# Kernel optimization log

Hardware: AMD Instinct MI355X
Metric: run time of the kernel (lower is better)

## Reference

```python
import jax, jax.numpy as jnp
import numpy as np

T_STEPS = 1000
TEMP_SAMPLE = 0.1


def _cosine_schedule():
    # matches MBDDegradationImputation._cosine_beta_schedule (float64 then cast)
    s = 0.008
    x = np.linspace(0, T_STEPS, T_STEPS + 1, dtype=np.float64)
    ac = np.cos((x / T_STEPS + s) / (1 + s) * np.pi * 0.5) ** 2
    ac = ac / ac[0]
    betas = np.clip(1.0 - ac[1:] / ac[:-1], 0.0, 0.999)
    alphas = 1.0 - betas
    acp = np.cumprod(alphas)
    return (jnp.asarray(alphas, jnp.float32),
            jnp.asarray(acp, jnp.float32),
            jnp.asarray(np.sqrt(1.0 - acp), jnp.float32))


def setup_inputs() -> dict:
    key = jax.random.key(0)
    k = jax.random.split(key, 6)
    N, T, F = 2048, 512, 64
    Xbar_i = jax.random.normal(k[0], (T, F), jnp.float32)
    observed_data = jax.random.normal(k[1], (T, F), jnp.float32)
    time_points = jnp.linspace(0.0, 1.0, T, dtype=jnp.float32)
    mask = jax.random.uniform(k[2], (T, F)) > 0.3  # True = observed
    eps = jax.random.normal(k[3], (N, T, F), jnp.float32)
    deg_a = jax.random.normal(k[4], (F,), jnp.float32) * 0.1
    deg_b = jax.random.normal(k[5], (F,), jnp.float32) * 0.1
    return {"Xbar_i": Xbar_i, "observed_data": observed_data,
            "time_points": time_points, "mask": mask, "eps": eps,
            "deg_a": deg_a, "deg_b": deg_b, "i": 500}


def reference(Xbar_i, observed_data, time_points, mask, eps, deg_a, deg_b, i):
    alphas, acp, sigmas = _cosine_schedule()
    abar_i = acp[i]
    sigma_i = sigmas[i]
    alpha_i = alphas[i]
    abar_im1 = acp[i - 1]

    Yi = jnp.sqrt(abar_i) * Xbar_i  # (T, F)
    # candidate clean samples, clipped, observed positions restored
    X0s = jnp.clip(eps * sigma_i + Xbar_i, -1.0, 1.0)  # (N, T, F)
    cand = jnp.where(mask[None], observed_data[None], X0s)  # (N, T, F)

    # linear degradation model consistency: pred = a + b * t, score = -MSE
    pred = deg_a[None, :] + deg_b[None, :] * time_points[:, None]  # (T, F)
    scores = -jnp.mean((cand - pred[None]) ** 2, axis=(1, 2))  # (N,)

    std = jnp.maximum(jnp.std(scores, ddof=1), 1e-4)  # torch.std is unbiased
    logp0 = (scores - jnp.mean(scores)) / std / TEMP_SAMPLE
    weights = jax.nn.softmax(logp0)  # (N,)

    weighted = jnp.einsum('n,ntf->tf', weights, X0s)  # (T, F)
    # per-feature: missing positions get weighted combo; fully-observed
    # features are copied from observed_data; observed positions of
    # partially-missing features stay zero (faithful to the torch loop)
    feat_all = jnp.all(mask, axis=0)  # (F,)
    Xbar = jnp.where(~mask, weighted,
                     jnp.where(feat_all[None, :], observed_data, 0.0))

    score = (-Yi + jnp.sqrt(abar_i) * Xbar) / (1.0 - abar_i)
    Xim1 = (Yi + (1.0 - abar_i) * score) / jnp.sqrt(alpha_i)
    Xbar_im1 = Xim1 / jnp.sqrt(abar_im1)
    Xbar_im1 = jnp.where(mask, observed_data, Xbar_im1)
    return Xbar_im1
```

## Files before the change

kernel.cpp:

```cpp
#include <hip/hip_runtime.h>

typedef __attribute__((ext_vector_type(4))) int   i32x4;
typedef __attribute__((ext_vector_type(4))) float f32x4;

#define TF    32768
#define TF4   8192
#define NS    2048
#define NG    32
#define WCUT  1e-9f

__device__ __forceinline__ i32x4 mload4(const void* mask, int isI32, int idx4) {
  if (isI32) return ((const i32x4*)mask)[idx4];
  unsigned int w = ((const unsigned int*)mask)[idx4];
  i32x4 r;
  r[0] = (int)(w & 0xFFu);
  r[1] = (int)((w >> 8) & 0xFFu);
  r[2] = (int)((w >> 16) & 0xFFu);
  r[3] = (int)((w >> 24) & 0xFFu);
  return r;
}

__device__ __forceinline__ double ac_fn(int t) {
  const double s = 0.008;
  double c = cos(((double)t / 1000.0 + s) / (1.0 + s) * 1.5707963267948966);
  return c * c;
}
__device__ __forceinline__ double alpha_fn(int t) {
  double beta = 1.0 - ac_fn(t + 1) / ac_fn(t);
  beta = beta < 0.0 ? 0.0 : (beta > 0.999 ? 0.999 : beta);
  return 1.0 - beta;
}

__launch_bounds__(256)
__global__ void k1_fused(const int* __restrict__ ip,
                         const unsigned int* __restrict__ maskw,
                         const float* __restrict__ timep,
                         const float* __restrict__ dega,
                         const float* __restrict__ degb,
                         const float* __restrict__ xbar,
                         const float* __restrict__ obs,
                         const void* __restrict__ mask,
                         float* __restrict__ wsc,
                         float* __restrict__ sc, float* __restrict__ xq,
                         float* __restrict__ pq) {
  const int tid = threadIdx.x;
  __shared__ int badsh;
  __shared__ double prod[256];
  __shared__ float ssig;
  __shared__ int sIsI32;
  if (tid == 0) badsh = 0;
  __syncthreads();
  int bad = 0;
  for (int k = tid; k < TF4; k += 256)
    if (maskw[k] > 1u) bad = 1;
  if (bad) atomicOr(&badsh, 1);

  const int i = ip[0];
  double p = 1.0;
  for (int t = tid; t < i; t += 256) p *= alpha_fn(t);
  prod[tid] = p;
  __syncthreads();
  for (int s = 128; s > 0; s >>= 1) {
    if (tid < s) prod[tid] *= prod[tid + s];
    __syncthreads();
  }
  if (tid == 0) {
    double acp_im1 = prod[0];
    double ai = alpha_fn(i);
    double acp_i = acp_im1 * ai;
    float sig = (float)sqrt(1.0 - acp_i);
    ssig = sig;
    sIsI32 = badsh ? 0 : 1;
    if (blockIdx.x == 0) {
      wsc[0] = sig;
      wsc[1] = (float)acp_i;
      wsc[2] = (float)ai;
      wsc[3] = (float)acp_im1;
      ((int*)wsc)[8] = badsh ? 0 : 1;
    }
  }
  __syncthreads();
  const float sig = ssig;
  const int isI32 = sIsI32;

  const int pos4 = blockIdx.x * 256 + tid;
  const int t  = pos4 >> 4;
  const int f0 = (pos4 << 2) & 63;
  const float tv = timep[t];
  f32x4 da = *(const f32x4*)(dega + f0);
  f32x4 db = *(const f32x4*)(degb + f0);
  f32x4 x  = ((const f32x4*)xbar)[pos4];
  f32x4 o  = ((const f32x4*)obs)[pos4];
  i32x4 m  = mload4(mask, isI32, pos4);

  f32x4 scv, xqv, pqv;
  #pragma unroll
  for (int c = 0; c < 4; ++c) {
    const float pr = fmaf(db[c], tv, da[c]);
    const bool mm = m[c] != 0;
    scv[c] = mm ? 0.f : sig;
    xqv[c] = mm ? 0.f : x[c];
    pqv[c] = mm ? (o[c] - pr) : pr;
  }
  ((f32x4*)sc)[pos4] = scv;
  ((f32x4*)xq)[pos4] = xqv;
  ((f32x4*)pq)[pos4] = pqv;
}

__launch_bounds__(256)
__global__ void k2_scores(const float* __restrict__ eps,
                          const float* __restrict__ sc,
                          const float* __restrict__ xq,
                          const float* __restrict__ pq,
                          double* __restrict__ pscore) {
  const int tid = threadIdx.x;
  const int n0 = blockIdx.x * 4;
  const int kq = blockIdx.y;
  const int kbeg = kq * (TF4 / 4);
  const f32x4* e4 = (const f32x4*)eps;
  const f32x4* sc4 = (const f32x4*)sc;
  const f32x4* xq4 = (const f32x4*)xq;
  const f32x4* pq4 = (const f32x4*)pq;

  double acc[4] = {0.0, 0.0, 0.0, 0.0};
  #pragma unroll 2
  for (int k = kbeg + tid; k < kbeg + TF4 / 4; k += 512) {
    const int k1 = k + 256;
    f32x4 sv0 = sc4[k],  xv0 = xq4[k],  pv0 = pq4[k];
    f32x4 sv1 = sc4[k1], xv1 = xq4[k1], pv1 = pq4[k1];
    #pragma unroll
    for (int r = 0; r < 4; ++r) {
      const size_t row = (size_t)(n0 + r) * TF4;
      f32x4 e0 = e4[row + k];
      f32x4 e1 = e4[row + k1];
      float s = 0.f;
      #pragma unroll
      for (int c = 0; c < 4; ++c) {
        float v = fmaf(e0[c], sv0[c], xv0[c]);
        v = fminf(fmaxf(v, -1.f), 1.f);
        float d = v - pv0[c];
        s = fmaf(d, d, s);
      }
      #pragma unroll
      for (int c = 0; c < 4; ++c) {
        float v = fmaf(e1[c], sv1[c], xv1[c]);
        v = fminf(fmaxf(v, -1.f), 1.f);
        float d = v - pv1[c];
        s = fmaf(d, d, s);
      }
      acc[r] += (double)s;
    }
  }
  __shared__ double red[4 * 256];
  #pragma unroll
  for (int r = 0; r < 4; ++r) red[r * 256 + tid] = acc[r];
  __syncthreads();
  for (int s = 128; s > 0; s >>= 1) {
    if (tid < s) {
      #pragma unroll
      for (int r = 0; r < 4; ++r) red[r * 256 + tid] += red[r * 256 + tid + s];
    }
    __syncthreads();
  }
  if (tid < 4) pscore[kq * NS + n0 + tid] = red[tid * 256];
}

__launch_bounds__(256)
__global__ void k3_softmax(const double* __restrict__ pscore,
                           float* __restrict__ wsc,
                           int* __restrict__ cidx, float* __restrict__ cw) {
  const int tid = threadIdx.x;
  __shared__ double red[256];

  float s[8];
  #pragma unroll
  for (int j = 0; j < 8; ++j) {
    int n = tid + 256 * j;
    double t = pscore[n] + pscore[NS + n] + pscore[2 * NS + n] + pscore[3 * NS + n];
    s[j] = -(float)(t * (1.0 / 32768.0));
  }
  double t = 0.0;
  #pragma unroll
  for (int j = 0; j < 8; ++j) t += (double)s[j];
  red[tid] = t; __syncthreads();
  for (int st = 128; st > 0; st >>= 1) { if (tid < st) red[tid] += red[tid + st]; __syncthreads(); }
  const float mean = (float)(red[0] * (1.0 / 2048.0));
  __syncthreads();
  double v = 0.0;
  #pragma unroll
  for (int j = 0; j < 8; ++j) { float d = s[j] - mean; v += (double)d * (double)d; }
  red[tid] = v; __syncthreads();
  for (int st = 128; st > 0; st >>= 1) { if (tid < st) red[tid] += red[tid + st]; __syncthreads(); }
  float stdv = (float)sqrt(red[0] / 2047.0);
  stdv = fmaxf(stdv, 1e-4f);
  const float inv = 10.0f / stdv;
  float lp[8];
  double mx = -1e300;
  #pragma unroll
  for (int j = 0; j < 8; ++j) { lp[j] = (s[j] - mean) * inv; mx = fmax(mx, (double)lp[j]); }
  __syncthreads();
  red[tid] = mx; __syncthreads();
  for (int st = 128; st > 0; st >>= 1) { if (tid < st) red[tid] = fmax(red[tid], red[tid + st]); __syncthreads(); }
  const float M = (float)red[0];
  __syncthreads();
  float ev[8]; double es = 0.0;
  #pragma unroll
  for (int j = 0; j < 8; ++j) { ev[j] = expf(lp[j] - M); es += (double)ev[j]; }
  red[tid] = es; __syncthreads();
  for (int st = 128; st > 0; st >>= 1) { if (tid < st) red[tid] += red[tid + st]; __syncthreads(); }
  const float invS = (float)(1.0 / red[0]);

  float w[8]; int keep[8]; int c = 0;
  #pragma unroll
  for (int j = 0; j < 8; ++j) {
    w[j] = ev[j] * invS;
    keep[j] = w[j] > WCUT;
    c += keep[j];
  }
  __shared__ int cnt[256];
  cnt[tid] = c; __syncthreads();
  for (int off = 1; off < 256; off <<= 1) {
    int vv = (tid >= off) ? cnt[tid - off] : 0;
    __syncthreads();
    cnt[tid] += vv;
    __syncthreads();
  }
  int base = cnt[tid] - c;
  #pragma unroll
  for (int j = 0; j < 8; ++j) {
    if (keep[j]) {
      cidx[base] = tid + 256 * j;
      cw[base] = w[j];
      ++base;
    }
  }
  if (tid == 255) ((int*)wsc)[9] = cnt[255];
}

__launch_bounds__(256)
__global__ void k4_weighted(const float* __restrict__ eps,
                            const int* __restrict__ cidx,
                            const float* __restrict__ cw,
                            const float* __restrict__ wsc,
                            const float* __restrict__ xbar,
                            float* __restrict__ partial) {
  const int tid = threadIdx.x;
  const int pos4 = blockIdx.x * 256 + tid;
  const int g = blockIdx.y;
  const int Nk = ((const int*)wsc)[9];
  const float sig = wsc[0];
  const f32x4* e4 = (const f32x4*)eps;
  f32x4 xf = ((const f32x4*)xbar)[pos4];
  f32x4 acc = {0.f, 0.f, 0.f, 0.f};
  int j = g;
  for (; j + NG < Nk; j += 2 * NG) {
    const float w0 = cw[j];
    const int   n0 = cidx[j];
    const float w1 = cw[j + NG];
    const int   n1 = cidx[j + NG];
    f32x4 e0 = e4[(size_t)n0 * TF4 + pos4];
    f32x4 e1 = e4[(size_t)n1 * TF4 + pos4];
    #pragma unroll
    for (int c = 0; c < 4; ++c) {
      float v = fmaf(e0[c], sig, xf[c]);
      v = fminf(fmaxf(v, -1.f), 1.f);
      acc[c] = fmaf(w0, v, acc[c]);
    }
    #pragma unroll
    for (int c = 0; c < 4; ++c) {
      float v = fmaf(e1[c], sig, xf[c]);
      v = fminf(fmaxf(v, -1.f), 1.f);
      acc[c] = fmaf(w1, v, acc[c]);
    }
  }
  for (; j < Nk; j += NG) {
    const float w = cw[j];
    const int n = cidx[j];
    f32x4 e = e4[(size_t)n * TF4 + pos4];
    #pragma unroll
    for (int c = 0; c < 4; ++c) {
      float v = fmaf(e[c], sig, xf[c]);
      v = fminf(fmaxf(v, -1.f), 1.f);
      acc[c] = fmaf(w, v, acc[c]);
    }
  }
  ((f32x4*)partial)[(size_t)g * TF4 + pos4] = acc;
}

__launch_bounds__(256)
__global__ void k5_final(const float* __restrict__ partial,
                         const float* __restrict__ xbar,
                         const float* __restrict__ obs,
                         const void* __restrict__ mask,
                         const float* __restrict__ wsc,
                         float* __restrict__ out) {
  const int pos4 = blockIdx.x * 256 + threadIdx.x;
  const f32x4* p4 = (const f32x4*)partial;
  f32x4 w = {0.f, 0.f, 0.f, 0.f};
  #pragma unroll
  for (int g = 0; g < NG; ++g) {
    f32x4 a = p4[(size_t)g * TF4 + pos4];
    #pragma unroll
    for (int c = 0; c < 4; ++c) w[c] += a[c];
  }
  const float abar = wsc[1];
  const float sa = sqrtf(abar);
  const float ra = 1.f / sqrtf(wsc[2]);
  const float rb = 1.f / sqrtf(wsc[3]);
  const int isI32 = ((const int*)wsc)[8];
  f32x4 xf = ((const f32x4*)xbar)[pos4];
  f32x4 ov = ((const f32x4*)obs)[pos4];
  i32x4 m = mload4(mask, isI32, pos4);
  f32x4 res;
  #pragma unroll
  for (int c = 0; c < 4; ++c) {
    const float Yi = sa * xf[c];
    const float scv = (-Yi + sa * w[c]) / (1.f - abar);
    const float xim1 = (Yi + (1.f - abar) * scv) * ra;
    res[c] = m[c] ? ov[c] : (xim1 * rb);
  }
  ((f32x4*)out)[pos4] = res;
}

extern "C" void kernel_launch(void* const* d_in, const int* in_sizes, int n_in,
                              void* d_out, int out_size, void* d_ws, size_t ws_size,
                              hipStream_t stream) {
  const float* Xbar  = (const float*)d_in[0];
  const float* obs   = (const float*)d_in[1];
  const float* timep = (const float*)d_in[2];
  const void*  mask  = d_in[3];
  const float* eps   = (const float*)d_in[4];
  const float* dega  = (const float*)d_in[5];
  const float* degb  = (const float*)d_in[6];
  const int*   ip    = (const int*)d_in[7];

  float* ws = (float*)d_ws;
  float*  wsc       = ws;
  float*  sc        = ws + 16;
  float*  xq        = sc + TF;
  float*  pq        = xq + TF;
  double* pscore    = (double*)(pq + TF);
  int*    cidx      = (int*)(pscore + 4 * NS);
  float*  cw        = (float*)(cidx + NS);
  float*  partial   = cw + NS;

  hipLaunchKernelGGL(k1_fused,   dim3(32),       dim3(256), 0, stream,
                     ip, (const unsigned int*)mask, timep, dega, degb,
                     Xbar, obs, mask, wsc, sc, xq, pq);
  hipLaunchKernelGGL(k2_scores,  dim3(NS/4, 4),  dim3(256), 0, stream,
                     eps, sc, xq, pq, pscore);
  hipLaunchKernelGGL(k3_softmax, dim3(1),        dim3(256), 0, stream,
                     pscore, wsc, cidx, cw);
  hipLaunchKernelGGL(k4_weighted,dim3(32, NG),   dim3(256), 0, stream,
                     eps, cidx, cw, wsc, Xbar, partial);
  hipLaunchKernelGGL(k5_final,   dim3(32),       dim3(256), 0, stream,
                     partial, Xbar, obs, mask, wsc, (float*)d_out);
}
```

Measured before the change: 71.38 us.

## Fuse prep into score kernel and softmax into weighted-sum kernel

Folds the per-position precompute (sigma, masked xbar, residual pred) into the score kernel, which now processes 8 sample rows per block, and removes the separate prep launch and its workspace arrays. The single-block softmax/compaction is recomputed redundantly inside every block of the weighted-sum kernel, with the candidate list held in shared memory, which removes two launches. The cost is that each of the 1024 score blocks reruns the schedule product and mask scan, and every weighted-sum block repeats the full softmax and prefix scan. It also adds 16KB of LDS per block in the weighted-sum kernel.

Result: slower. 73.30 us (+2.7%).

```diff
diff --git a/kernel.cpp b/kernel.cpp
--- a/kernel.cpp
+++ b/kernel.cpp
@@ -6,6 +6,7 @@
 #define TF    32768
 #define TF4   8192
 #define NS    2048
+#define ROWS  8
 #define NG    32
 #define WCUT  1e-9f
 
@@ -31,23 +32,24 @@
   return 1.0 - beta;
 }
 
-__launch_bounds__(256)
-__global__ void k1_fused(const int* __restrict__ ip,
-                         const unsigned int* __restrict__ maskw,
-                         const float* __restrict__ timep,
-                         const float* __restrict__ dega,
-                         const float* __restrict__ degb,
-                         const float* __restrict__ xbar,
-                         const float* __restrict__ obs,
-                         const void* __restrict__ mask,
-                         float* __restrict__ wsc,
-                         float* __restrict__ sc, float* __restrict__ xq,
-                         float* __restrict__ pq) {
+__launch_bounds__(256, 4)
+__global__ void k12_scores(const int* __restrict__ ip,
+                           const unsigned int* __restrict__ maskw,
+                           const float* __restrict__ timep,
+                           const float* __restrict__ dega,
+                           const float* __restrict__ degb,
+                           const float* __restrict__ xbar,
+                           const float* __restrict__ obs,
+                           const void* __restrict__ mask,
+                           const float* __restrict__ eps,
+                           float* __restrict__ wsc,
+                           double* __restrict__ pscore) {
   const int tid = threadIdx.x;
+  __shared__ double red[ROWS * 256];
   __shared__ int badsh;
-  __shared__ double prod[256];
   __shared__ float ssig;
   __shared__ int sIsI32;
+
   if (tid == 0) badsh = 0;
   __syncthreads();
   int bad = 0;
@@ -58,20 +60,20 @@
   const int i = ip[0];
   double p = 1.0;
   for (int t = tid; t < i; t += 256) p *= alpha_fn(t);
-  prod[tid] = p;
+  red[tid] = p;
   __syncthreads();
   for (int s = 128; s > 0; s >>= 1) {
-    if (tid < s) prod[tid] *= prod[tid + s];
+    if (tid < s) red[tid] *= red[tid + s];
     __syncthreads();
   }
   if (tid == 0) {
-    double acp_im1 = prod[0];
+    double acp_im1 = red[0];
     double ai = alpha_fn(i);
     double acp_i = acp_im1 * ai;
     float sig = (float)sqrt(1.0 - acp_i);
     ssig = sig;
     sIsI32 = badsh ? 0 : 1;
-    if (blockIdx.x == 0) {
+    if (blockIdx.x == 0 && blockIdx.y == 0) {
       wsc[0] = sig;
       wsc[1] = (float)acp_i;
       wsc[2] = (float)ai;
@@ -83,94 +85,73 @@
   const float sig = ssig;
   const int isI32 = sIsI32;
 
-  const int pos4 = blockIdx.x * 256 + tid;
-  const int t  = pos4 >> 4;
-  const int f0 = (pos4 << 2) & 63;
-  const float tv = timep[t];
-  f32x4 da = *(const f32x4*)(dega + f0);
-  f32x4 db = *(const f32x4*)(degb + f0);
-  f32x4 x  = ((const f32x4*)xbar)[pos4];
-  f32x4 o  = ((const f32x4*)obs)[pos4];
-  i32x4 m  = mload4(mask, isI32, pos4);
-
-  f32x4 scv, xqv, pqv;
-  #pragma unroll
-  for (int c = 0; c < 4; ++c) {
-    const float pr = fmaf(db[c], tv, da[c]);
-    const bool mm = m[c] != 0;
-    scv[c] = mm ? 0.f : sig;
-    xqv[c] = mm ? 0.f : x[c];
-    pqv[c] = mm ? (o[c] - pr) : pr;
-  }
-  ((f32x4*)sc)[pos4] = scv;
-  ((f32x4*)xq)[pos4] = xqv;
-  ((f32x4*)pq)[pos4] = pqv;
-}
-
-__launch_bounds__(256)
-__global__ void k2_scores(const float* __restrict__ eps,
-                          const float* __restrict__ sc,
-                          const float* __restrict__ xq,
-                          const float* __restrict__ pq,
-                          double* __restrict__ pscore) {
-  const int tid = threadIdx.x;
-  const int n0 = blockIdx.x * 4;
+  const int n0 = blockIdx.x * ROWS;
   const int kq = blockIdx.y;
   const int kbeg = kq * (TF4 / 4);
   const f32x4* e4 = (const f32x4*)eps;
-  const f32x4* sc4 = (const f32x4*)sc;
-  const f32x4* xq4 = (const f32x4*)xq;
-  const f32x4* pq4 = (const f32x4*)pq;
-
-  double acc[4] = {0.0, 0.0, 0.0, 0.0};
+  const f32x4* x4 = (const f32x4*)xbar;
+  const f32x4* o4 = (const f32x4*)obs;
+
+  double acc[ROWS];
+  #pragma unroll
+  for (int r = 0; r < ROWS; ++r) acc[r] = 0.0;
+
   #pragma unroll 2
-  for (int k = kbeg + tid; k < kbeg + TF4 / 4; k += 512) {
-    const int k1 = k + 256;
-    f32x4 sv0 = sc4[k],  xv0 = xq4[k],  pv0 = pq4[k];
-    f32x4 sv1 = sc4[k1], xv1 = xq4[k1], pv1 = pq4[k1];
-    #pragma unroll
-    for (int r = 0; r < 4; ++r) {
-      const size_t row = (size_t)(n0 + r) * TF4;
-      f32x4 e0 = e4[row + k];
-      f32x4 e1 = e4[row + k1];
+  for (int k = kbeg + tid; k < kbeg + TF4 / 4; k += 256) {
+    f32x4 x = x4[k], o = o4[k];
+    i32x4 m = mload4(mask, isI32, k);
+    const int t  = k >> 4;
+    const int f0 = (k << 2) & 63;
+    const float tv = timep[t];
+    f32x4 da = *(const f32x4*)(dega + f0);
+    f32x4 db = *(const f32x4*)(degb + f0);
+    f32x4 sv, xv, pv;
+    #pragma unroll
+    for (int c = 0; c < 4; ++c) {
+      const float pr = fmaf(db[c], tv, da[c]);
+      const bool mm = m[c] != 0;
+      sv[c] = mm ? 0.f : sig;
+      xv[c] = mm ? 0.f : x[c];
+      pv[c] = mm ? (o[c] - pr) : pr;
+    }
+    #pragma unroll
+    for (int r = 0; r < ROWS; ++r) {
+      f32x4 e = e4[(size_t)(n0 + r) * TF4 + k];
       float s = 0.f;
       #pragma unroll
       for (int c = 0; c < 4; ++c) {
-        float v = fmaf(e0[c], sv0[c], xv0[c]);
+        float v = fmaf(e[c], sv[c], xv[c]);
         v = fminf(fmaxf(v, -1.f), 1.f);
-        float d = v - pv0[c];
-        s = fmaf(d, d, s);
-      }
-      #pragma unroll
-      for (int c = 0; c < 4; ++c) {
-        float v = fmaf(e1[c], sv1[c], xv1[c]);
-        v = fminf(fmaxf(v, -1.f), 1.f);
-        float d = v - pv1[c];
+        float d = v - pv[c];
         s = fmaf(d, d, s);
       }
       acc[r] += (double)s;
     }
   }
-  __shared__ double red[4 * 256];
-  #pragma unroll
-  for (int r = 0; r < 4; ++r) red[r * 256 + tid] = acc[r];
+  #pragma unroll
+  for (int r = 0; r < ROWS; ++r) red[r * 256 + tid] = acc[r];
   __syncthreads();
   for (int s = 128; s > 0; s >>= 1) {
     if (tid < s) {
       #pragma unroll
-      for (int r = 0; r < 4; ++r) red[r * 256 + tid] += red[r * 256 + tid + s];
+      for (int r = 0; r < ROWS; ++r) red[r * 256 + tid] += red[r * 256 + tid + s];
     }
     __syncthreads();
   }
-  if (tid < 4) pscore[kq * NS + n0 + tid] = red[tid * 256];
+  if (tid < ROWS) pscore[kq * NS + n0 + tid] = red[tid * 256];
 }
 
 __launch_bounds__(256)
-__global__ void k3_softmax(const double* __restrict__ pscore,
-                           float* __restrict__ wsc,
-                           int* __restrict__ cidx, float* __restrict__ cw) {
+__global__ void k34_weighted(const double* __restrict__ pscore,
+                             const float* __restrict__ eps,
+                             const float* __restrict__ xbar,
+                             const float* __restrict__ wsc,
+                             float* __restrict__ partial) {
   const int tid = threadIdx.x;
   __shared__ double red[256];
+  __shared__ int cnt[256];
+  __shared__ int   ciL[NS];
+  __shared__ float cwL[NS];
 
   float s[8];
   #pragma unroll
@@ -217,7 +198,6 @@
     keep[j] = w[j] > WCUT;
     c += keep[j];
   }
-  __shared__ int cnt[256];
   cnt[tid] = c; __syncthreads();
   for (int off = 1; off < 256; off <<= 1) {
     int vv = (tid >= off) ? cnt[tid - off] : 0;
@@ -229,59 +209,50 @@
   #pragma unroll
   for (int j = 0; j < 8; ++j) {
     if (keep[j]) {
-      cidx[base] = tid + 256 * j;
-      cw[base] = w[j];
+      ciL[base] = tid + 256 * j;
+      cwL[base] = w[j];
       ++base;
     }
   }
-  if (tid == 255) ((int*)wsc)[9] = cnt[255];
-}
-
-__launch_bounds__(256)
-__global__ void k4_weighted(const float* __restrict__ eps,
-                            const int* __restrict__ cidx,
-                            const float* __restrict__ cw,
-                            const float* __restrict__ wsc,
-                            const float* __restrict__ xbar,
-                            float* __restrict__ partial) {
-  const int tid = threadIdx.x;
+  const int Nk = cnt[255];
+  __syncthreads();
+
   const int pos4 = blockIdx.x * 256 + tid;
   const int g = blockIdx.y;
-  const int Nk = ((const int*)wsc)[9];
   const float sig = wsc[0];
   const f32x4* e4 = (const f32x4*)eps;
   f32x4 xf = ((const f32x4*)xbar)[pos4];
   f32x4 acc = {0.f, 0.f, 0.f, 0.f};
   int j = g;
   for (; j + NG < Nk; j += 2 * NG) {
-    const float w0 = cw[j];
-    const int   n0 = cidx[j];
-    const float w1 = cw[j + NG];
-    const int   n1 = cidx[j + NG];
+    const float w0 = cwL[j];
+    const int   n0 = ciL[j];
+    const float w1 = cwL[j + NG];
+    const int   n1 = ciL[j + NG];
     f32x4 e0 = e4[(size_t)n0 * TF4 + pos4];
     f32x4 e1 = e4[(size_t)n1 * TF4 + pos4];
     #pragma unroll
-    for (int c = 0; c < 4; ++c) {
-      float v = fmaf(e0[c], sig, xf[c]);
-      v = fminf(fmaxf(v, -1.f), 1.f);
-      acc[c] = fmaf(w0, v, acc[c]);
-    }
-    #pragma unroll
-    for (int c = 0; c < 4; ++c) {
-      float v = fmaf(e1[c], sig, xf[c]);
-      v = fminf(fmaxf(v, -1.f), 1.f);
-      acc[c] = fmaf(w1, v, acc[c]);
+    for (int c2 = 0; c2 < 4; ++c2) {
+      float vv = fmaf(e0[c2], sig, xf[c2]);
+      vv = fminf(fmaxf(vv, -1.f), 1.f);
+      acc[c2] = fmaf(w0, vv, acc[c2]);
+    }
+    #pragma unroll
+    for (int c2 = 0; c2 < 4; ++c2) {
+      float vv = fmaf(e1[c2], sig, xf[c2]);
+      vv = fminf(fmaxf(vv, -1.f), 1.f);
+      acc[c2] = fmaf(w1, vv, acc[c2]);
     }
   }
   for (; j < Nk; j += NG) {
-    const float w = cw[j];
-    const int n = cidx[j];
+    const float ww = cwL[j];
+    const int n = ciL[j];
     f32x4 e = e4[(size_t)n * TF4 + pos4];
     #pragma unroll
-    for (int c = 0; c < 4; ++c) {
-      float v = fmaf(e[c], sig, xf[c]);
-      v = fminf(fmaxf(v, -1.f), 1.f);
-      acc[c] = fmaf(w, v, acc[c]);
+    for (int c2 = 0; c2 < 4; ++c2) {
+      float vv = fmaf(e[c2], sig, xf[c2]);
+      vv = fminf(fmaxf(vv, -1.f), 1.f);
+      acc[c2] = fmaf(ww, vv, acc[c2]);
     }
   }
   ((f32x4*)partial)[(size_t)g * TF4 + pos4] = acc;
@@ -297,7 +268,7 @@
   const int pos4 = blockIdx.x * 256 + threadIdx.x;
   const f32x4* p4 = (const f32x4*)partial;
   f32x4 w = {0.f, 0.f, 0.f, 0.f};
-  #pragma unroll
+  #pragma unroll 8
   for (int g = 0; g < NG; ++g) {
     f32x4 a = p4[(size_t)g * TF4 + pos4];
     #pragma unroll
@@ -335,24 +306,15 @@
   const int*   ip    = (const int*)d_in[7];
 
   float* ws = (float*)d_ws;
-  float*  wsc       = ws;
-  float*  sc        = ws + 16;
-  float*  xq        = sc + TF;
-  float*  pq        = xq + TF;
-  double* pscore    = (double*)(pq + TF);
-  int*    cidx      = (int*)(pscore + 4 * NS);
-  float*  cw        = (float*)(cidx + NS);
-  float*  partial   = cw + NS;
-
-  hipLaunchKernelGGL(k1_fused,   dim3(32),       dim3(256), 0, stream,
+  float*  wsc     = ws;
+  double* pscore  = (double*)(ws + 16);
+  float*  partial = (float*)(pscore + 4 * NS);
+
+  hipLaunchKernelGGL(k12_scores, dim3(NS/ROWS, 4), dim3(256), 0, stream,
                      ip, (const unsigned int*)mask, timep, dega, degb,
-                     Xbar, obs, mask, wsc, sc, xq, pq);
-  hipLaunchKernelGGL(k2_scores,  dim3(NS/4, 4),  dim3(256), 0, stream,
-                     eps, sc, xq, pq, pscore);
-  hipLaunchKernelGGL(k3_softmax, dim3(1),        dim3(256), 0, stream,
-                     pscore, wsc, cidx, cw);
-  hipLaunchKernelGGL(k4_weighted,dim3(32, NG),   dim3(256), 0, stream,
-                     eps, cidx, cw, wsc, Xbar, partial);
-  hipLaunchKernelGGL(k5_final,   dim3(32),       dim3(256), 0, stream,
+                     Xbar, obs, mask, eps, wsc, pscore);
+  hipLaunchKernelGGL(k34_weighted, dim3(32, NG),   dim3(256), 0, stream,
+                     pscore, eps, Xbar, wsc, partial);
+  hipLaunchKernelGGL(k5_final,     dim3(32),       dim3(256), 0, stream,
                      partial, Xbar, obs, mask, wsc, (float*)d_out);
 }
```

## Fuse softmax candidate selection into weighted-sum kernel, redundantly per block

Applied to the files above, without the earlier changes.

The single-block softmax/compaction kernel is merged into the weighted-accumulation kernel. Each of the 32x32 blocks now recomputes the 2048-score normalization, softmax, and prefix-sum compaction into shared memory, so one launch and the global round trip of the index/weight lists go away. The cost is 1024 copies of the reduction work, each with many syncthreads and 8KB of pscore reads (cache-resident), plus more shared memory per block. The final reduction loop unroll is also capped at 8.

Measured after the change: 71.39 us. Within noise of the previous version (+0.0%).

```diff
diff --git a/kernel.cpp b/kernel.cpp
--- a/kernel.cpp
+++ b/kernel.cpp
@@ -166,11 +166,16 @@
 }
 
 __launch_bounds__(256)
-__global__ void k3_softmax(const double* __restrict__ pscore,
-                           float* __restrict__ wsc,
-                           int* __restrict__ cidx, float* __restrict__ cw) {
+__global__ void k34_weighted(const double* __restrict__ pscore,
+                             const float* __restrict__ eps,
+                             const float* __restrict__ xbar,
+                             const float* __restrict__ wsc,
+                             float* __restrict__ partial) {
   const int tid = threadIdx.x;
   __shared__ double red[256];
+  __shared__ int cnt[256];
+  __shared__ int   ciL[NS];
+  __shared__ float cwL[NS];
 
   float s[8];
   #pragma unroll
@@ -217,7 +222,6 @@
     keep[j] = w[j] > WCUT;
     c += keep[j];
   }
-  __shared__ int cnt[256];
   cnt[tid] = c; __syncthreads();
   for (int off = 1; off < 256; off <<= 1) {
     int vv = (tid >= off) ? cnt[tid - off] : 0;
@@ -229,59 +233,50 @@
   #pragma unroll
   for (int j = 0; j < 8; ++j) {
     if (keep[j]) {
-      cidx[base] = tid + 256 * j;
-      cw[base] = w[j];
+      ciL[base] = tid + 256 * j;
+      cwL[base] = w[j];
       ++base;
     }
   }
-  if (tid == 255) ((int*)wsc)[9] = cnt[255];
-}
-
-__launch_bounds__(256)
-__global__ void k4_weighted(const float* __restrict__ eps,
-                            const int* __restrict__ cidx,
-                            const float* __restrict__ cw,
-                            const float* __restrict__ wsc,
-                            const float* __restrict__ xbar,
-                            float* __restrict__ partial) {
-  const int tid = threadIdx.x;
+  const int Nk = cnt[255];
+  __syncthreads();
+
   const int pos4 = blockIdx.x * 256 + tid;
   const int g = blockIdx.y;
-  const int Nk = ((const int*)wsc)[9];
   const float sig = wsc[0];
   const f32x4* e4 = (const f32x4*)eps;
   f32x4 xf = ((const f32x4*)xbar)[pos4];
   f32x4 acc = {0.f, 0.f, 0.f, 0.f};
   int j = g;
   for (; j + NG < Nk; j += 2 * NG) {
-    const float w0 = cw[j];
-    const int   n0 = cidx[j];
-    const float w1 = cw[j + NG];
-    const int   n1 = cidx[j + NG];
+    const float w0 = cwL[j];
+    const int   n0 = ciL[j];
+    const float w1 = cwL[j + NG];
+    const int   n1 = ciL[j + NG];
     f32x4 e0 = e4[(size_t)n0 * TF4 + pos4];
     f32x4 e1 = e4[(size_t)n1 * TF4 + pos4];
     #pragma unroll
-    for (int c = 0; c < 4; ++c) {
-      float v = fmaf(e0[c], sig, xf[c]);
-      v = fminf(fmaxf(v, -1.f), 1.f);
-      acc[c] = fmaf(w0, v, acc[c]);
-    }
-    #pragma unroll
-    for (int c = 0; c < 4; ++c) {
-      float v = fmaf(e1[c], sig, xf[c]);
-      v = fminf(fmaxf(v, -1.f), 1.f);
-      acc[c] = fmaf(w1, v, acc[c]);
+    for (int c2 = 0; c2 < 4; ++c2) {
+      float vv = fmaf(e0[c2], sig, xf[c2]);
+      vv = fminf(fmaxf(vv, -1.f), 1.f);
+      acc[c2] = fmaf(w0, vv, acc[c2]);
+    }
+    #pragma unroll
+    for (int c2 = 0; c2 < 4; ++c2) {
+      float vv = fmaf(e1[c2], sig, xf[c2]);
+      vv = fminf(fmaxf(vv, -1.f), 1.f);
+      acc[c2] = fmaf(w1, vv, acc[c2]);
     }
   }
   for (; j < Nk; j += NG) {
-    const float w = cw[j];
-    const int n = cidx[j];
+    const float ww = cwL[j];
+    const int n = ciL[j];
     f32x4 e = e4[(size_t)n * TF4 + pos4];
     #pragma unroll
-    for (int c = 0; c < 4; ++c) {
-      float v = fmaf(e[c], sig, xf[c]);
-      v = fminf(fmaxf(v, -1.f), 1.f);
-      acc[c] = fmaf(w, v, acc[c]);
+    for (int c2 = 0; c2 < 4; ++c2) {
+      float vv = fmaf(e[c2], sig, xf[c2]);
+      vv = fminf(fmaxf(vv, -1.f), 1.f);
+      acc[c2] = fmaf(ww, vv, acc[c2]);
     }
   }
   ((f32x4*)partial)[(size_t)g * TF4 + pos4] = acc;
@@ -297,7 +292,7 @@
   const int pos4 = blockIdx.x * 256 + threadIdx.x;
   const f32x4* p4 = (const f32x4*)partial;
   f32x4 w = {0.f, 0.f, 0.f, 0.f};
-  #pragma unroll
+  #pragma unroll 8
   for (int g = 0; g < NG; ++g) {
     f32x4 a = p4[(size_t)g * TF4 + pos4];
     #pragma unroll
@@ -335,24 +330,20 @@
   const int*   ip    = (const int*)d_in[7];
 
   float* ws = (float*)d_ws;
-  float*  wsc       = ws;
-  float*  sc        = ws + 16;
-  float*  xq        = sc + TF;
-  float*  pq        = xq + TF;
-  double* pscore    = (double*)(pq + TF);
-  int*    cidx      = (int*)(pscore + 4 * NS);
-  float*  cw        = (float*)(cidx + NS);
-  float*  partial   = cw + NS;
+  float*  wsc     = ws;
+  float*  sc      = ws + 16;
+  float*  xq      = sc + TF;
+  float*  pq      = xq + TF;
+  double* pscore  = (double*)(pq + TF);
+  float*  partial = (float*)(pscore + 4 * NS);
 
   hipLaunchKernelGGL(k1_fused,   dim3(32),       dim3(256), 0, stream,
                      ip, (const unsigned int*)mask, timep, dega, degb,
                      Xbar, obs, mask, wsc, sc, xq, pq);
   hipLaunchKernelGGL(k2_scores,  dim3(NS/4, 4),  dim3(256), 0, stream,
                      eps, sc, xq, pq, pscore);
-  hipLaunchKernelGGL(k3_softmax, dim3(1),        dim3(256), 0, stream,
-                     pscore, wsc, cidx, cw);
-  hipLaunchKernelGGL(k4_weighted,dim3(32, NG),   dim3(256), 0, stream,
-                     eps, cidx, cw, wsc, Xbar, partial);
-  hipLaunchKernelGGL(k5_final,   dim3(32),       dim3(256), 0, stream,
+  hipLaunchKernelGGL(k34_weighted, dim3(32, NG), dim3(256), 0, stream,
+                     pscore, eps, Xbar, wsc, partial);
+  hipLaunchKernelGGL(k5_final,     dim3(32),     dim3(256), 0, stream,
                      partial, Xbar, obs, mask, wsc, (float*)d_out);
 }
```
